# Kernel tuning notes

Hardware: AMD Instinct MI355X
Metric: run time of the kernel (lower is better)

Reference implementation:

```python
import jax, jax.numpy as jnp
import numpy as np

B, C, H, W = 2, 128, 96, 96
HEADS, DHEAD, WIN = 4, 32, 5
INNER = HEADS * DHEAD
PAD = WIN // 2


def setup_inputs() -> dict:
    key = jax.random.key(0)
    k1, k2, k3, k4, k5 = jax.random.split(key, 5)
    s = 1.0 / np.sqrt(C)
    return {
        "x": jax.random.normal(k1, (B, C, H, W), dtype=jnp.float32),
        "wq": jax.random.normal(k2, (INNER, C), dtype=jnp.float32) * s,
        "wk": jax.random.normal(k3, (INNER, C), dtype=jnp.float32) * s,
        "wv": jax.random.normal(k4, (INNER, C), dtype=jnp.float32) * s,
        "wproj": jax.random.normal(k5, (C, INNER), dtype=jnp.float32) * s,
    }


def _windows(t):
    # same neighborhood ordering as F.unfold (row-major over kernel offsets).
    tp = jnp.pad(t, ((0, 0), (0, 0), (0, 0), (PAD, PAD), (PAD, PAD)))
    wins = [tp[:, :, :, di:di + H, dj:dj + W]
            for di in range(WIN) for dj in range(WIN)]
    return jnp.stack(wins, axis=3)


def reference(x, wq, wk, wv, wproj):
    # 1x1 convs == per-pixel linear maps
    q = jnp.einsum('oc,bcxy->boxy', wq, x).reshape(B, HEADS, DHEAD, H, W)
    k = jnp.einsum('oc,bcxy->boxy', wk, x).reshape(B, HEADS, DHEAD, H, W)
    v = jnp.einsum('oc,bcxy->boxy', wv, x).reshape(B, HEADS, DHEAD, H, W)

    k_win = _windows(k)  # (B,h,d,25,H,W)
    v_win = _windows(v)

    scale = 1.0 / np.sqrt(DHEAD)
    attn = jnp.einsum('bhdxy,bhdkxy->bhkxy', q, k_win) * scale
    attn = jax.nn.softmax(attn, axis=2)  # softmax over the 25 window positions
    out = jnp.einsum('bhkxy,bhdkxy->bhdxy', attn, v_win)

    out = out.reshape(B, INNER, H, W)
    return jnp.einsum('co,boxy->bcxy', wproj, out)
```

## Files before the change

### kernel.cpp

```cpp
#include <hip/hip_runtime.h>
#include <hip/hip_fp16.h>

#define PP 9216

typedef _Float16 f16x8 __attribute__((ext_vector_type(8)));
typedef _Float16 f16x4 __attribute__((ext_vector_type(4)));
typedef _Float16 h2    __attribute__((ext_vector_type(2)));
typedef float    f32x4 __attribute__((ext_vector_type(4)));

#define LDS_BYTES 32768

__device__ __forceinline__ int swz128(int row, int hc) {
    return row * 128 + (((hc >> 3) ^ (row & 15)) << 3) + (hc & 7);
}
__device__ __forceinline__ int swz64(int row, int hc) {
    return row * 64 + (((hc >> 3) ^ (row & 7)) << 3) + (hc & 7);
}

__global__ __launch_bounds__(256) void prep_w(
    const float* __restrict__ wq, const float* __restrict__ wk,
    const float* __restrict__ wv, const float* __restrict__ wp,
    _Float16* __restrict__ wqkv16, _Float16* __restrict__ wp16)
{
    int e = (blockIdx.x * 256 + threadIdx.x) * 4;
    const float* src;
    _Float16* dst;
    if (e < 49152) {
        int o = e >> 7;
        src = (o < 128) ? (wq + (size_t)o * 128)
            : (o < 256) ? (wk + (size_t)(o - 128) * 128)
                        : (wv + (size_t)(o - 256) * 128);
        src += (e & 127);
        dst = wqkv16 + e;
    } else {
        int j = e - 49152;
        src = wp + j;
        dst = wp16 + j;
    }
    float4 v = *(const float4*)src;
    f16x4 h;
    h[0] = (_Float16)v.x; h[1] = (_Float16)v.y;
    h[2] = (_Float16)v.z; h[3] = (_Float16)v.w;
    *(f16x4*)dst = h;
}

__global__ __launch_bounds__(256, 4) void fused_attn(
    const float* __restrict__ x, const _Float16* __restrict__ wqkv,
    const _Float16* __restrict__ wp16, float* __restrict__ out)
{
    __shared__ __align__(16) char smem[LDS_BYTES];
    _Float16* sA = (_Float16*)smem;
    _Float16* sB = (_Float16*)(smem + 16384);

    const int t = threadIdx.x;
    const int w = t >> 6, lane = t & 63, lm = lane & 15, quad = lane >> 4;

    const int wgid = (blockIdx.x & 7) * 144 + (blockIdx.x >> 3);
    const int b = wgid / 576;
    const int rem = wgid - b * 576;
    const int x0 = (rem % 24) * 4, y0 = (rem / 24) * 4;

    const float* xb = x + (size_t)b * 128 * PP;
    float* ob = out + (size_t)b * 128 * PP;

    f16x8 BKV[4][4];
    #pragma unroll
    for (int ni = 0; ni < 4; ni++) {
        const int wrow = (ni < 2) ? (128 + (w + 4 * ni) * 16 + lm)
                                  : (256 + (2 * w + (ni - 2)) * 16 + lm);
        const _Float16* wr = wqkv + (size_t)wrow * 128;
        #pragma unroll
        for (int kc = 0; kc < 4; kc++)
            BKV[ni][kc] = *(const f16x8*)(wr + kc * 32 + quad * 8);
    }

    {
        const int pos = (t & 31) * 2;
        const int gy = y0 - 2 + (pos >> 3);
        const int gx = x0 - 2 + (pos & 7);
        const bool inb = ((unsigned)gy < 96u) && ((unsigned)gx < 96u);
        const float* src = xb + (size_t)(t >> 5) * PP + gy * 96 + gx;
        float2 vv[16];
        #pragma unroll
        for (int i = 0; i < 16; i++)
            vv[i] = inb ? *(const float2*)(src + (size_t)(i * 8) * PP)
                        : make_float2(0.f, 0.f);
        #pragma unroll
        for (int i = 0; i < 16; i++) {
            int c = i * 8 + (t >> 5);
            sA[swz128(pos,     c)] = (_Float16)vv[i].x;
            sA[swz128(pos + 1, c)] = (_Float16)vv[i].y;
        }
    }
    __syncthreads();

    h2 vpk[2][4][2];
    #pragma unroll
    for (int m = 0; m < 4; m++) {
        f16x8 A[4];
        #pragma unroll
        for (int kc = 0; kc < 4; kc++)
            A[kc] = *(const f16x8*)(sA + swz128(m * 16 + lm, kc * 32 + quad * 8));
        #pragma unroll
        for (int ni = 0; ni < 4; ni++) {
            f32x4 acc = {0.f, 0.f, 0.f, 0.f};
            #pragma unroll
            for (int kc = 0; kc < 4; kc++)
                acc = __builtin_amdgcn_mfma_f32_16x16x32_f16(
                    A[kc], BKV[ni][kc], acc, 0, 0, 0);
            if (ni < 2) {
                int n = w + 4 * ni;
                #pragma unroll
                for (int r = 0; r < 4; r++)
                    sB[swz128(m * 16 + quad * 4 + r, n * 16 + lm)] = (_Float16)acc[r];
            } else {
                h2 p0, p1;
                p0[0] = (_Float16)acc[0]; p0[1] = (_Float16)acc[1];
                p1[0] = (_Float16)acc[2]; p1[1] = (_Float16)acc[3];
                vpk[ni - 2][m][0] = p0;
                vpk[ni - 2][m][1] = p1;
            }
        }
    }

    f16x8 A3[4];
    {
        int hrow = ((lm >> 2) + 2) * 8 + (lm & 3) + 2;
        #pragma unroll
        for (int kc = 0; kc < 4; kc++)
            A3[kc] = *(const f16x8*)(sA + swz128(hrow, kc * 32 + quad * 8));
    }

    f16x8 BQ[2][4];
    #pragma unroll
    for (int nn = 0; nn < 2; nn++) {
        const _Float16* wr = wqkv + (size_t)((2 * w + nn) * 16 + lm) * 128;
        #pragma unroll
        for (int kc = 0; kc < 4; kc++)
            BQ[nn][kc] = *(const f16x8*)(wr + kc * 32 + quad * 8);
    }
    __syncthreads();

    _Float16* sQ = sA + 4608;
    #pragma unroll
    for (int nn = 0; nn < 2; nn++) {
        f32x4 acc = {0.f, 0.f, 0.f, 0.f};
        #pragma unroll
        for (int kc = 0; kc < 4; kc++)
            acc = __builtin_amdgcn_mfma_f32_16x16x32_f16(
                A3[kc], BQ[nn][kc], acc, 0, 0, 0);
        #pragma unroll
        for (int r = 0; r < 4; r++)
            sQ[swz128(quad * 4 + r, (2 * w + nn) * 16 + lm)] = (_Float16)acc[r];
    }

    f32x4 S[4];
    {
        f16x8 Aq = *(const f16x8*)(sQ + swz128(lm, w * 32 + quad * 8));
        #pragma unroll
        for (int n = 0; n < 4; n++) {
            f16x8 Bk = *(const f16x8*)(sB + swz128(n * 16 + lm, w * 32 + quad * 8));
            f32x4 z = {0.f, 0.f, 0.f, 0.f};
            S[n] = __builtin_amdgcn_mfma_f32_16x16x32_f16(Aq, Bk, z, 0, 0, 0);
        }
    }

    _Float16* sPh = sA + w * 1152;
    float inv4[4];
    {
        const float scale = 0.17677669529663689f;
        #pragma unroll
        for (int r = 0; r < 4; r++) {
            float e[4];
            float mx = -1e30f;
            #pragma unroll
            for (int n = 0; n < 4; n++) {
                int hy = n * 2 + (lm >> 3), hx = lm & 7;
                bool memb = (hy >= quad) && (hy < quad + 5) && (hx >= r) && (hx < r + 5);
                e[n] = memb ? S[n][r] * scale : -1e30f;
                mx = fmaxf(mx, e[n]);
            }
            mx = fmaxf(mx, __shfl_xor(mx, 1));
            mx = fmaxf(mx, __shfl_xor(mx, 2));
            mx = fmaxf(mx, __shfl_xor(mx, 4));
            mx = fmaxf(mx, __shfl_xor(mx, 8));
            float sum = 0.f;
            #pragma unroll
            for (int n = 0; n < 4; n++) {
                float ev = __expf(e[n] - mx);
                e[n] = ev;
                sum += ev;
            }
            sum += __shfl_xor(sum, 1);
            sum += __shfl_xor(sum, 2);
            sum += __shfl_xor(sum, 4);
            sum += __shfl_xor(sum, 8);
            inv4[r] = 1.f / sum;
            #pragma unroll
            for (int n = 0; n < 4; n++)
                sPh[(quad * 4 + r) * 72 + n * 16 + lm] = (_Float16)e[n];
        }
    }

    f16x8 Aw[2][4];
    #pragma unroll
    for (int mi = 0; mi < 2; mi++) {
        const _Float16* wr = wp16 + (size_t)((w * 2 + mi) * 16 + lm) * 128;
        #pragma unroll
        for (int kc = 0; kc < 4; kc++)
            Aw[mi][kc] = *(const f16x8*)(wr + kc * 32 + quad * 8);
    }
    __syncthreads();

    _Float16* sVh = sB + w * 2048;
    #pragma unroll
    for (int nn = 0; nn < 2; nn++)
        #pragma unroll
        for (int m = 0; m < 4; m++)
            #pragma unroll
            for (int rp = 0; rp < 2; rp++)
                *(h2*)(sVh + swz64(nn * 16 + lm, m * 16 + quad * 4 + rp * 2))
                    = vpk[nn][m][rp];

    _Float16* sAo = sQ;
    {
        f16x8 Ap[2];
        #pragma unroll
        for (int kc = 0; kc < 2; kc++)
            Ap[kc] = *(const f16x8*)(sPh + lm * 72 + kc * 32 + quad * 8);
        #pragma unroll
        for (int nd = 0; nd < 2; nd++) {
            f32x4 acc = {0.f, 0.f, 0.f, 0.f};
            #pragma unroll
            for (int kc = 0; kc < 2; kc++) {
                f16x8 Bv = *(const f16x8*)(sVh + swz64(nd * 16 + lm, kc * 32 + quad * 8));
                acc = __builtin_amdgcn_mfma_f32_16x16x32_f16(Ap[kc], Bv, acc, 0, 0, 0);
            }
            #pragma unroll
            for (int r = 0; r < 4; r++)
                sAo[swz128(quad * 4 + r, w * 32 + nd * 16 + lm)] =
                    (_Float16)(acc[r] * inv4[r]);
        }
    }
    __syncthreads();

    {
        f16x8 Bf[4];
        #pragma unroll
        for (int kc = 0; kc < 4; kc++)
            Bf[kc] = *(const f16x8*)(sAo + swz128(lm, kc * 32 + quad * 8));
        int gp = (y0 + (lm >> 2)) * 96 + x0 + (lm & 3);
        #pragma unroll
        for (int mi = 0; mi < 2; mi++) {
            f32x4 acc = {0.f, 0.f, 0.f, 0.f};
            #pragma unroll
            for (int kc = 0; kc < 4; kc++)
                acc = __builtin_amdgcn_mfma_f32_16x16x32_f16(
                    Aw[mi][kc], Bf[kc], acc, 0, 0, 0);
            int c0 = (w * 2 + mi) * 16 + quad * 4;
            #pragma unroll
            for (int r = 0; r < 4; r++)
                ob[(size_t)(c0 + r) * PP + gp] = acc[r];
        }
    }
}

extern "C" void kernel_launch(void* const* d_in, const int* in_sizes, int n_in,
                              void* d_out, int out_size, void* d_ws, size_t ws_size,
                              hipStream_t stream)
{
    const float* x  = (const float*)d_in[0];
    const float* wq = (const float*)d_in[1];
    const float* wk = (const float*)d_in[2];
    const float* wv = (const float*)d_in[3];
    const float* wp = (const float*)d_in[4];
    float* out = (float*)d_out;

    _Float16* wqkv16 = (_Float16*)d_ws;
    _Float16* wp16   = wqkv16 + 49152;

    prep_w<<<dim3(64), 256, 0, stream>>>(wq, wk, wv, wp, wqkv16, wp16);
    fused_attn<<<dim3(1152), 256, 0, stream>>>(x, wqkv16, wp16, out);
}
```

Before: 106.7 us.

## Shrink LDS footprint by aliasing buffers and staging V in halves

Result: slower. 116.4 us (+9.0%).

```diff
diff --git a/kernel.cpp b/kernel.cpp
--- a/kernel.cpp
+++ b/kernel.cpp
@@ -8,13 +8,16 @@
 typedef _Float16 h2    __attribute__((ext_vector_type(2)));
 typedef float    f32x4 __attribute__((ext_vector_type(4)));
 
-#define LDS_BYTES 32768
+#define LDS_BYTES 20480
 
 __device__ __forceinline__ int swz128(int row, int hc) {
     return row * 128 + (((hc >> 3) ^ (row & 15)) << 3) + (hc & 7);
 }
 __device__ __forceinline__ int swz64(int row, int hc) {
     return row * 64 + (((hc >> 3) ^ (row & 7)) << 3) + (hc & 7);
+}
+__device__ __forceinline__ int swz32(int row, int hc) {
+    return row * 32 + (((hc >> 3) ^ (row & 3)) << 3) + (hc & 7);
 }
 
 __global__ __launch_bounds__(256) void prep_w(
@@ -49,8 +52,8 @@
     const _Float16* __restrict__ wp16, float* __restrict__ out)
 {
     __shared__ __align__(16) char smem[LDS_BYTES];
-    _Float16* sA = (_Float16*)smem;
-    _Float16* sB = (_Float16*)(smem + 16384);
+    _Float16* sXK = (_Float16*)smem;
+    _Float16* sQ  = (_Float16*)(smem + 16384);
 
     const int t = threadIdx.x;
     const int w = t >> 6, lane = t & 63, lm = lane & 15, quad = lane >> 4;
@@ -88,11 +91,19 @@
         #pragma unroll
         for (int i = 0; i < 16; i++) {
             int c = i * 8 + (t >> 5);
-            sA[swz128(pos,     c)] = (_Float16)vv[i].x;
-            sA[swz128(pos + 1, c)] = (_Float16)vv[i].y;
-        }
-    }
-    __syncthreads();
+            sXK[swz128(pos,     c)] = (_Float16)vv[i].x;
+            sXK[swz128(pos + 1, c)] = (_Float16)vv[i].y;
+        }
+    }
+    __syncthreads();
+
+    f16x8 A3[4];
+    {
+        int hrow = ((lm >> 2) + 2) * 8 + (lm & 3) + 2;
+        #pragma unroll
+        for (int kc = 0; kc < 4; kc++)
+            A3[kc] = *(const f16x8*)(sXK + swz128(hrow, kc * 32 + quad * 8));
+    }
 
     h2 vpk[2][4][2];
     #pragma unroll
@@ -100,7 +111,8 @@
         f16x8 A[4];
         #pragma unroll
         for (int kc = 0; kc < 4; kc++)
-            A[kc] = *(const f16x8*)(sA + swz128(m * 16 + lm, kc * 32 + quad * 8));
+            A[kc] = *(const f16x8*)(sXK + swz128(m * 16 + lm, kc * 32 + quad * 8));
+        __syncthreads();
         #pragma unroll
         for (int ni = 0; ni < 4; ni++) {
             f32x4 acc = {0.f, 0.f, 0.f, 0.f};
@@ -112,7 +124,7 @@
                 int n = w + 4 * ni;
                 #pragma unroll
                 for (int r = 0; r < 4; r++)
-                    sB[swz128(m * 16 + quad * 4 + r, n * 16 + lm)] = (_Float16)acc[r];
+                    sXK[swz128(m * 16 + quad * 4 + r, n * 16 + lm)] = (_Float16)acc[r];
             } else {
                 h2 p0, p1;
                 p0[0] = (_Float16)acc[0]; p0[1] = (_Float16)acc[1];
@@ -123,14 +135,6 @@
         }
     }
 
-    f16x8 A3[4];
-    {
-        int hrow = ((lm >> 2) + 2) * 8 + (lm & 3) + 2;
-        #pragma unroll
-        for (int kc = 0; kc < 4; kc++)
-            A3[kc] = *(const f16x8*)(sA + swz128(hrow, kc * 32 + quad * 8));
-    }
-
     f16x8 BQ[2][4];
     #pragma unroll
     for (int nn = 0; nn < 2; nn++) {
@@ -141,7 +145,6 @@
     }
     __syncthreads();
 
-    _Float16* sQ = sA + 4608;
     #pragma unroll
     for (int nn = 0; nn < 2; nn++) {
         f32x4 acc = {0.f, 0.f, 0.f, 0.f};
@@ -159,13 +162,14 @@
         f16x8 Aq = *(const f16x8*)(sQ + swz128(lm, w * 32 + quad * 8));
         #pragma unroll
         for (int n = 0; n < 4; n++) {
-            f16x8 Bk = *(const f16x8*)(sB + swz128(n * 16 + lm, w * 32 + quad * 8));
+            f16x8 Bk = *(const f16x8*)(sXK + swz128(n * 16 + lm, w * 32 + quad * 8));
             f32x4 z = {0.f, 0.f, 0.f, 0.f};
             S[n] = __builtin_amdgcn_mfma_f32_16x16x32_f16(Aq, Bk, z, 0, 0, 0);
         }
     }
-
-    _Float16* sPh = sA + w * 1152;
+    __syncthreads();
+
+    _Float16* sPh = (_Float16*)(smem + w * 2048);
     float inv4[4];
     {
         const float scale = 0.17677669529663689f;
@@ -198,7 +202,7 @@
             inv4[r] = 1.f / sum;
             #pragma unroll
             for (int n = 0; n < 4; n++)
-                sPh[(quad * 4 + r) * 72 + n * 16 + lm] = (_Float16)e[n];
+                sPh[swz64(quad * 4 + r, n * 16 + lm)] = (_Float16)e[n];
         }
     }
 
@@ -210,37 +214,34 @@
         for (int kc = 0; kc < 4; kc++)
             Aw[mi][kc] = *(const f16x8*)(wr + kc * 32 + quad * 8);
     }
-    __syncthreads();
-
-    _Float16* sVh = sB + w * 2048;
-    #pragma unroll
-    for (int nn = 0; nn < 2; nn++)
-        #pragma unroll
-        for (int m = 0; m < 4; m++)
-            #pragma unroll
-            for (int rp = 0; rp < 2; rp++)
-                *(h2*)(sVh + swz64(nn * 16 + lm, m * 16 + quad * 4 + rp * 2))
-                    = vpk[nn][m][rp];
-
+
+    _Float16* sVh = (_Float16*)(smem + 8192 + w * 2048);
     _Float16* sAo = sQ;
     {
-        f16x8 Ap[2];
-        #pragma unroll
-        for (int kc = 0; kc < 2; kc++)
-            Ap[kc] = *(const f16x8*)(sPh + lm * 72 + kc * 32 + quad * 8);
-        #pragma unroll
-        for (int nd = 0; nd < 2; nd++) {
-            f32x4 acc = {0.f, 0.f, 0.f, 0.f};
-            #pragma unroll
-            for (int kc = 0; kc < 2; kc++) {
-                f16x8 Bv = *(const f16x8*)(sVh + swz64(nd * 16 + lm, kc * 32 + quad * 8));
-                acc = __builtin_amdgcn_mfma_f32_16x16x32_f16(Ap[kc], Bv, acc, 0, 0, 0);
-            }
+        f32x4 acc2[2] = {{0.f, 0.f, 0.f, 0.f}, {0.f, 0.f, 0.f, 0.f}};
+        #pragma unroll
+        for (int h = 0; h < 2; h++) {
+            #pragma unroll
+            for (int nn = 0; nn < 2; nn++)
+                #pragma unroll
+                for (int mm = 0; mm < 2; mm++)
+                    #pragma unroll
+                    for (int rp = 0; rp < 2; rp++)
+                        *(h2*)(sVh + swz32(nn * 16 + lm, mm * 16 + quad * 4 + rp * 2))
+                            = vpk[nn][2 * h + mm][rp];
+            f16x8 Ap = *(const f16x8*)(sPh + swz64(lm, h * 32 + quad * 8));
+            #pragma unroll
+            for (int nd = 0; nd < 2; nd++) {
+                f16x8 Bv = *(const f16x8*)(sVh + swz32(nd * 16 + lm, quad * 8));
+                acc2[nd] = __builtin_amdgcn_mfma_f32_16x16x32_f16(Ap, Bv, acc2[nd], 0, 0, 0);
+            }
+        }
+        #pragma unroll
+        for (int nd = 0; nd < 2; nd++)
             #pragma unroll
             for (int r = 0; r < 4; r++)
                 sAo[swz128(quad * 4 + r, w * 32 + nd * 16 + lm)] =
-                    (_Float16)(acc[r] * inv4[r]);
-        }
+                    (_Float16)(acc2[nd][r] * inv4[r]);
     }
     __syncthreads();
 
```
